# Optimization experiments

Measured on AMD Instinct MI355X. Metric: run time of the kernel, lower is better.

The kernel has to match this reference:

```python
import jax, jax.numpy as jnp
import numpy as np

DIM = 768
HEADS = 12
HIDDEN = 4 * DIM
EPS = 1e-5


def _layernorm(x, g, b):
    mu = jnp.mean(x, axis=-1, keepdims=True)
    var = jnp.var(x, axis=-1, keepdims=True)
    return (x - mu) * jax.lax.rsqrt(var + EPS) * g + b


def setup_inputs() -> dict:
    key = jax.random.key(0)
    ks = jax.random.split(key, 8)
    B, N, C = 16, 577, DIM
    s = lambda fan: 1.0 / np.sqrt(fan)
    return {
        "x": jax.random.normal(ks[0], (B, N, C), jnp.float32),
        "ln1_g": jnp.ones((C,), jnp.float32),
        "ln1_b": jnp.zeros((C,), jnp.float32),
        "qkv_w": jax.random.normal(ks[1], (C, 3 * C), jnp.float32) * s(C),
        "qkv_b": jnp.zeros((3 * C,), jnp.float32),
        "proj_w": jax.random.normal(ks[2], (C, C), jnp.float32) * s(C),
        "proj_b": jnp.zeros((C,), jnp.float32),
        "ln2_g": jnp.ones((C,), jnp.float32),
        "ln2_b": jnp.zeros((C,), jnp.float32),
        "fc1_w": jax.random.normal(ks[3], (C, HIDDEN), jnp.float32) * s(C),
        "fc1_b": jnp.zeros((HIDDEN,), jnp.float32),
        "fc2_w": jax.random.normal(ks[4], (HIDDEN, C), jnp.float32) * s(HIDDEN),
        "fc2_b": jnp.zeros((C,), jnp.float32),
    }


def reference(x, ln1_g, ln1_b, qkv_w, qkv_b, proj_w, proj_b,
              ln2_g, ln2_b, fc1_w, fc1_b, fc2_w, fc2_b):
    B, N, C = x.shape
    H = HEADS
    Dh = C // H
    scale = Dh ** (-0.5)

    # --- attention branch (pre-norm) ---
    xn = _layernorm(x, ln1_g, ln1_b)
    qkv = xn @ qkv_w + qkv_b                         # [B,N,3C]
    qkv = qkv.reshape(B, N, 3, H, Dh).transpose(2, 0, 3, 1, 4)  # [3,B,H,N,Dh]
    q, k, v = qkv[0], qkv[1], qkv[2]
    attn = jax.nn.softmax(jnp.einsum('bhnd,bhmd->bhnm', q, k) * scale, axis=-1)
    y = jnp.einsum('bhnm,bhmd->bhnd', attn, v)       # [B,H,N,Dh]
    y = y.transpose(0, 2, 1, 3).reshape(B, N, C)
    y = y @ proj_w + proj_b
    x = x + y

    # --- MLP branch (pre-norm, exact GELU as torch default) ---
    xn2 = _layernorm(x, ln2_g, ln2_b)
    h = jax.nn.gelu(xn2 @ fc1_w + fc1_b, approximate=False)
    x = x + (h @ fc2_w + fc2_b)
    return x
```

## Files before the change

### kernel.cpp

```cpp
#include <hip/hip_runtime.h>
#include <hip/hip_bf16.h>
#include <math.h>


#define C_DIM   768
#define SEQ     577
#define BATCH   16
#define NHEAD   12
#define DHEAD   64
#define MREAL   (BATCH*SEQ)
#define MPAD    9472
#define HID     3072
#define QKW     1536
#define NKV     640
#define QSCALE  0.1803368801111204f

typedef __hip_bfloat16 bf16;
typedef __attribute__((ext_vector_type(8))) short v8s;
typedef __attribute__((ext_vector_type(4))) float v4f;
typedef __attribute__((ext_vector_type(16))) float v16f;

static __device__ __forceinline__ bf16 f2b(float f){ return __float2bfloat16(f); }
static __device__ __forceinline__ float us2f(unsigned short u){
  union{ float f; unsigned int i; } x; x.i = ((unsigned int)u)<<16; return x.f;
}
static __device__ __forceinline__ short f2s(float f){
  bf16 t = __float2bfloat16(f); return *(short*)&t;
}
static __device__ __forceinline__ float gelu_fast(float x){
  float z2 = 2.302585092994046f * x * (1.f + 0.044715f*x*x);
  return x / (1.f + exp2f(-z2));
}

__global__ __launch_bounds__(256) void k_transpose_all(
    const float* __restrict__ qkvw, const float* __restrict__ projw,
    const float* __restrict__ fc1w, const float* __restrict__ fc2w,
    bf16* __restrict__ qkvT, bf16* __restrict__ projT,
    bf16* __restrict__ fc1T, bf16* __restrict__ fc2T)
{
  int id = blockIdx.x;
  const float* src; bf16* dst; int R, C, nx;
  if (id < 432)      { src=qkvw; dst=qkvT; R=768;  C=2304; nx=36; }
  else if (id < 576) { id-=432; src=projw; dst=projT; R=768;  C=768;  nx=12; }
  else if (id < 1152){ id-=576; src=fc1w;  dst=fc1T;  R=768;  C=3072; nx=48; }
  else               { id-=1152; src=fc2w; dst=fc2T;  R=3072; C=768;  nx=12; }
  const int tr = (id/nx)*64, tc = (id%nx)*64;

  __shared__ float s[64][65];
  const int t = threadIdx.x;
  const int lr = t >> 4, lc4 = t & 15;
  #pragma unroll
  for (int i=0;i<4;i++){
    int r = lr + i*16;
    float4 v = *(const float4*)(src + (size_t)(tr+r)*C + tc + lc4*4);
    s[r][lc4*4+0]=v.x; s[r][lc4*4+1]=v.y; s[r][lc4*4+2]=v.z; s[r][lc4*4+3]=v.w;
  }
  __syncthreads();
  const int c = t >> 2, seg = t & 3;
  alignas(16) bf16 tmp[16];
  #pragma unroll
  for (int j=0;j<16;j++) tmp[j] = f2b(s[seg*16+j][c]);
  bf16* dp = dst + (size_t)(tc+c)*R + tr + seg*16;
  *(uint4*)dp       = *(uint4*)tmp;
  *(uint4*)(dp + 8) = *(uint4*)(tmp + 8);
}

__global__ __launch_bounds__(256) void k_layernorm(
    const float* __restrict__ in, const float* __restrict__ g,
    const float* __restrict__ b, bf16* __restrict__ o)
{
  int row = blockIdx.x, tid = threadIdx.x;
  size_t base = (size_t)row*C_DIM;
  if (row >= MREAL){
    #pragma unroll
    for (int j=0;j<3;j++) o[base + tid + j*256] = f2b(0.f);
    return;
  }
  float v[3], s=0.f, ss=0.f;
  #pragma unroll
  for (int j=0;j<3;j++){ v[j] = in[base + tid + j*256]; s += v[j]; ss += v[j]*v[j]; }
  #pragma unroll
  for (int off=32; off>0; off>>=1){ s += __shfl_xor(s,off); ss += __shfl_xor(ss,off); }
  __shared__ float red[8];
  int wv = tid>>6;
  if ((tid&63)==0){ red[wv] = s; red[4+wv] = ss; }
  __syncthreads();
  float S  = red[0]+red[1]+red[2]+red[3];
  float SS = red[4]+red[5]+red[6]+red[7];
  float mu   = S*(1.f/C_DIM);
  float rstd = rsqrtf(SS*(1.f/C_DIM) - mu*mu + 1e-5f);
  #pragma unroll
  for (int j=0;j<3;j++){
    int c = tid + j*256;
    o[base+c] = f2b((v[j]-mu)*rstd*g[c] + b[c]);
  }
}

__global__ __launch_bounds__(256) void k_reduce2_ln(
    const bf16* __restrict__ P, const float* __restrict__ bias,
    const float* __restrict__ resid, float* __restrict__ out,
    const float* __restrict__ g, const float* __restrict__ bln,
    bf16* __restrict__ xn2)
{
  int row = blockIdx.x, tid = threadIdx.x;
  size_t base = (size_t)row*C_DIM;
  if (row >= MREAL){
    #pragma unroll
    for (int j=0;j<3;j++) xn2[base + tid + j*256] = f2b(0.f);
    return;
  }
  const unsigned short* P0 = (const unsigned short*)P;
  const unsigned short* P1 = P0 + (size_t)MPAD*C_DIM;
  float v[3], s=0.f, ss=0.f;
  #pragma unroll
  for (int j=0;j<3;j++){
    int c = tid + j*256;
    size_t idx = base + c;
    float val = us2f(P0[idx]) + us2f(P1[idx]) + bias[c] + resid[idx];
    out[idx] = val; v[j] = val; s += val; ss += val*val;
  }
  #pragma unroll
  for (int off=32; off>0; off>>=1){ s += __shfl_xor(s,off); ss += __shfl_xor(ss,off); }
  __shared__ float red[8];
  int wv = tid>>6;
  if ((tid&63)==0){ red[wv] = s; red[4+wv] = ss; }
  __syncthreads();
  float S  = red[0]+red[1]+red[2]+red[3];
  float SS = red[4]+red[5]+red[6]+red[7];
  float mu   = S*(1.f/C_DIM);
  float rstd = rsqrtf(SS*(1.f/C_DIM) - mu*mu + 1e-5f);
  #pragma unroll
  for (int j=0;j<3;j++){
    int c = tid + j*256;
    xn2[base+c] = f2b((v[j]-mu)*rstd*g[c] + bln[c]);
  }
}

__global__ __launch_bounds__(256) void k_reduce2(
    const bf16* __restrict__ P, const float* __restrict__ bias,
    const float* __restrict__ resid, float* __restrict__ out)
{
  size_t i = ((size_t)blockIdx.x*256 + threadIdx.x)*8;
  int c = (int)(i % C_DIM);
  v8s p0 = *(const v8s*)(P + i);
  v8s p1 = *(const v8s*)(P + (size_t)MPAD*C_DIM + i);
  float r[8];
  #pragma unroll
  for (int j=0;j<8;j++) r[j] = resid[i+j];
  #pragma unroll
  for (int j=0;j<8;j++)
    out[i+j] = us2f((unsigned short)p0[j]) + us2f((unsigned short)p1[j])
             + bias[c+j] + r[j];
}

__global__ __launch_bounds__(256, 3) void k_flash(
    const bf16* __restrict__ qk, const bf16* __restrict__ VtAll,
    bf16* __restrict__ y)
{
  __shared__ alignas(16) bf16 sK[2][64*64];
  __shared__ alignas(16) bf16 sV[2][64*64];
  __shared__ alignas(16) bf16 sP[4][16*72];

  const int tid = threadIdx.x;
  const int wave = tid>>6, lane = tid&63;
  const int r16 = lane&15, kg = lane>>4;

  const int id = blockIdx.x;
  const int swz = (id&7)*240 + (id>>3);
  const int hh = swz/10, qt = swz - hh*10;
  const int b_ = hh/NHEAD, h_ = hh - b_*NHEAD;

  const int qrow = b_*SEQ + qt*64 + wave*16 + r16;
  v8s qf[2];
  qf[0] = *(const v8s*)(qk + (size_t)qrow*QKW + h_*DHEAD + kg*8);
  qf[1] = *(const v8s*)(qk + (size_t)qrow*QKW + h_*DHEAD + 32 + kg*8);

  auto stage = [&](int kt, int buf){
    #pragma unroll
    for (int i=0;i<2;i++){
      int chunk = i*256 + tid;
      int row = chunk>>3, ch = chunk&7;
      int sc = ch ^ (row&7);
      const bf16* gk = qk + (size_t)(b_*SEQ + kt*64 + row)*QKW
                          + C_DIM + h_*DHEAD + sc*8;
      const bf16* gv = VtAll + (size_t)(b_*C_DIM + h_*DHEAD + row)*NKV
                             + kt*64 + sc*8;
      __builtin_amdgcn_global_load_lds(
          (const __attribute__((address_space(1))) void*)gk,
          (__attribute__((address_space(3))) void*)((char*)&sK[buf][0] + i*4096 + wave*1024),
          16, 0, 0);
      __builtin_amdgcn_global_load_lds(
          (const __attribute__((address_space(1))) void*)gv,
          (__attribute__((address_space(3))) void*)((char*)&sV[buf][0] + i*4096 + wave*1024),
          16, 0, 0);
    }
  };

  float m_run = -1e30f, l_run = 0.f;
  v4f zero4 = {0.f,0.f,0.f,0.f};
  v4f o[4] = {zero4, zero4, zero4, zero4};

  stage(0, 0);
  for (int kt=0; kt<10; ++kt){
    __syncthreads();
    if (kt < 9) stage(kt+1, (kt+1)&1);
    const bf16* Kt = &sK[kt&1][0];
    const bf16* Vt = &sV[kt&1][0];

    v4f sfr[4] = {zero4, zero4, zero4, zero4};
    #pragma unroll
    for (int ks=0; ks<2; ++ks){
      #pragma unroll
      for (int m=0;m<4;m++){
        int key = m*16 + r16;
        v8s kf = *(const v8s*)(Kt + key*64 + (((ks*4+kg) ^ (key&7))*8));
        sfr[m] = __builtin_amdgcn_mfma_f32_16x16x32_bf16(kf, qf[ks], sfr[m], 0, 0, 0);
      }
    }

    if (kt == 9){
      #pragma unroll
      for (int m=0;m<4;m++)
        #pragma unroll
        for (int gg=0; gg<4; ++gg){
          int kb = 576 + m*16 + kg*4 + gg;
          if (kb >= SEQ) sfr[m][gg] = -1e30f;
        }
    }

    float tmax = -1e30f;
    #pragma unroll
    for (int m=0;m<4;m++)
      #pragma unroll
      for (int gg=0; gg<4; ++gg) tmax = fmaxf(tmax, sfr[m][gg]);
    tmax = fmaxf(tmax, __shfl_xor(tmax, 16));
    tmax = fmaxf(tmax, __shfl_xor(tmax, 32));
    float mn  = fmaxf(m_run, tmax);
    float scl = exp2f(m_run - mn);
    float ps  = 0.f;
    #pragma unroll
    for (int m=0;m<4;m++)
      #pragma unroll
      for (int gg=0; gg<4; ++gg){
        float pv = exp2f(sfr[m][gg] - mn);
        sfr[m][gg] = pv; ps += pv;
      }
    ps += __shfl_xor(ps, 16);
    ps += __shfl_xor(ps, 32);
    l_run = l_run*scl + ps;
    m_run = mn;
    #pragma unroll
    for (int mf=0; mf<4; ++mf) o[mf] *= scl;

    bf16* Pw = &sP[wave][0];
    #pragma unroll
    for (int m=0;m<4;m++){
      short4 w;
      w.x = f2s(sfr[m][0]); w.y = f2s(sfr[m][1]);
      w.z = f2s(sfr[m][2]); w.w = f2s(sfr[m][3]);
      *(short4*)(Pw + r16*72 + m*16 + kg*4) = w;
    }
    asm volatile("s_waitcnt lgkmcnt(0)" ::: "memory");
    v8s pb0 = *(const v8s*)(Pw + r16*72 + kg*8);
    v8s pb1 = *(const v8s*)(Pw + r16*72 + 32 + kg*8);
    #pragma unroll
    for (int mf=0; mf<4; ++mf){
      int d = mf*16 + r16;
      v8s v0 = *(const v8s*)(Vt + d*64 + ((kg     ^ (d&7))*8));
      v8s v1 = *(const v8s*)(Vt + d*64 + (((4+kg) ^ (d&7))*8));
      o[mf] = __builtin_amdgcn_mfma_f32_16x16x32_bf16(v0, pb0, o[mf], 0, 0, 0);
      o[mf] = __builtin_amdgcn_mfma_f32_16x16x32_bf16(v1, pb1, o[mf], 0, 0, 0);
    }
  }

  const int qg = qt*64 + wave*16 + r16;
  if (qg < SEQ){
    float inv = 1.f / l_run;
    #pragma unroll
    for (int mf=0; mf<4; ++mf){
      short4 w;
      w.x = f2s(o[mf][0]*inv); w.y = f2s(o[mf][1]*inv);
      w.z = f2s(o[mf][2]*inv); w.w = f2s(o[mf][3]*inv);
      *(short4*)(y + (size_t)(b_*SEQ + qg)*C_DIM + h_*DHEAD + mf*16 + kg*4) = w;
    }
  }
}

template<int EPI>
__global__ __launch_bounds__(256, 4) void gemm_bt(
    const bf16* __restrict__ A, int lda,
    const bf16* __restrict__ BT, int ldb,
    void* Cv, int ldc,
    const float* __restrict__ bias,
    const float* resid,
    int K)
{
  __shared__ alignas(16) bf16 sA[128*64];
  __shared__ alignas(16) bf16 sB[128*64];
  const int tid  = threadIdx.x;
  const int wave = tid>>6, lane = tid&63;
  const int wr = wave>>1, wc = wave&1;
  const int r16 = lane&15, kg = lane>>4;

  int nx = gridDim.x, nwg = nx*gridDim.y;
  int id = blockIdx.y*nx + blockIdx.x;
  int qq = nwg>>3, r8 = nwg&7, xcd = id&7, j = id>>3;
  int swz = (xcd<r8 ? xcd*(qq+1) : r8*(qq+1) + (xcd-r8)*qq) + j;
  int mt = swz / nx, nt = swz % nx;

  int kb = 0;
  if constexpr (EPI==6) kb = blockIdx.z * K;

  v4f acc[4][4];
  v4f zero4 = {0.f,0.f,0.f,0.f};
  #pragma unroll
  for (int m=0;m<4;m++)
    #pragma unroll
    for (int n=0;n<4;n++) acc[m][n] = zero4;

  const int mrow0 = mt*128, ncol0 = nt*128;

  for (int kt=0; kt<K; kt+=64){
    #pragma unroll
    for (int i=0;i<4;i++){
      int ci = wave*4 + i;
      int q  = ci*64 + lane;
      int rr = q>>3;
      int cc = (q&7)*8;
      const bf16* ga = A  + (size_t)(mrow0+rr)*lda + (kb+kt+cc);
      const bf16* gb = BT + (size_t)(ncol0+rr)*ldb + (kb+kt+cc);
      __builtin_amdgcn_global_load_lds(
          (const __attribute__((address_space(1))) void*)ga,
          (__attribute__((address_space(3))) void*)((char*)sA + ci*1024), 16, 0, 0);
      __builtin_amdgcn_global_load_lds(
          (const __attribute__((address_space(1))) void*)gb,
          (__attribute__((address_space(3))) void*)((char*)sB + ci*1024), 16, 0, 0);
    }
    __syncthreads();
    #pragma unroll
    for (int ks=0; ks<2; ks++){
      v8s av[4], bv[4];
      #pragma unroll
      for (int m=0;m<4;m++)
        av[m] = *(const v8s*)(sA + (wr*64 + m*16 + r16)*64 + ks*32 + kg*8);
      #pragma unroll
      for (int n=0;n<4;n++)
        bv[n] = *(const v8s*)(sB + (wc*64 + n*16 + r16)*64 + ks*32 + kg*8);
      #pragma unroll
      for (int m=0;m<4;m++)
        #pragma unroll
        for (int n=0;n<4;n++)
          acc[m][n] = __builtin_amdgcn_mfma_f32_16x16x32_bf16(av[m], bv[n], acc[m][n], 0, 0, 0);
    }
    __syncthreads();
  }

  #pragma unroll
  for (int m=0;m<4;m++){
    #pragma unroll
    for (int n=0;n<4;n++){
      int col = ncol0 + wc*64 + n*16 + r16;
      #pragma unroll
      for (int gg=0; gg<4; gg++){
        int row = mrow0 + wr*64 + m*16 + kg*4 + gg;
        float v = acc[m][n][gg];
        if constexpr (EPI==0){
          float oo = v + bias[col];
          if (col < C_DIM) oo *= QSCALE;
          ((bf16*)Cv)[(size_t)row*ldc + col] = f2b(oo);
        } else if constexpr (EPI==5){
          int g = col;
          if (g < MREAL){
            int b = g / SEQ;
            int key = g - b*SEQ;
            ((bf16*)Cv)[((size_t)b*C_DIM + row)*NKV + key] = f2b(v + bias[row]);
          }
        } else {
          ((bf16*)Cv)[(size_t)blockIdx.z*MPAD*C_DIM + (size_t)row*ldc + col] = f2b(v);
        }
      }
    }
  }
}

__global__ __launch_bounds__(256, 4) void gemm_bt32(
    const bf16* __restrict__ A, int lda,
    const bf16* __restrict__ BT, int ldb,
    bf16* __restrict__ Cv, int ldc,
    const float* __restrict__ bias,
    int K)
{
  __shared__ alignas(16) bf16 sA[128*64];
  __shared__ alignas(16) bf16 sB[128*64];
  const int tid  = threadIdx.x;
  const int wave = tid>>6, lane = tid&63;
  const int wr = wave>>1, wc = wave&1;
  const int l31 = lane&31, lh = lane>>5;

  int nx = gridDim.x, nwg = nx*gridDim.y;
  int id = blockIdx.y*nx + blockIdx.x;
  int qq = nwg>>3, r8 = nwg&7, xcd = id&7, j = id>>3;
  int swz = (xcd<r8 ? xcd*(qq+1) : r8*(qq+1) + (xcd-r8)*qq) + j;
  int mt = swz / nx, nt = swz % nx;
  const int mrow0 = mt*128, ncol0 = nt*128;

  v16f acc[2][2];
  #pragma unroll
  for (int i=0;i<2;i++)
    #pragma unroll
    for (int jn=0;jn<2;jn++)
      #pragma unroll
      for (int r=0;r<16;r++) acc[i][jn][r] = 0.f;

  for (int kt=0; kt<K; kt+=64){
    #pragma unroll
    for (int i=0;i<4;i++){
      int ci = wave*4 + i;
      int q  = ci*64 + lane;
      int rr = q>>3;
      int cc = (q&7)*8;
      const bf16* ga = A  + (size_t)(mrow0+rr)*lda + (kt+cc);
      const bf16* gb = BT + (size_t)(ncol0+rr)*ldb + (kt+cc);
      __builtin_amdgcn_global_load_lds(
          (const __attribute__((address_space(1))) void*)ga,
          (__attribute__((address_space(3))) void*)((char*)sA + ci*1024), 16, 0, 0);
      __builtin_amdgcn_global_load_lds(
          (const __attribute__((address_space(1))) void*)gb,
          (__attribute__((address_space(3))) void*)((char*)sB + ci*1024), 16, 0, 0);
    }
    __syncthreads();
    #pragma unroll
    for (int ks=0; ks<4; ks++){
      v8s a[2], b[2];
      #pragma unroll
      for (int i=0;i<2;i++)
        a[i] = *(const v8s*)(sA + (wr*64 + i*32 + l31)*64 + ks*16 + lh*8);
      #pragma unroll
      for (int jn=0;jn<2;jn++)
        b[jn] = *(const v8s*)(sB + (wc*64 + jn*32 + l31)*64 + ks*16 + lh*8);
      #pragma unroll
      for (int i=0;i<2;i++)
        #pragma unroll
        for (int jn=0;jn<2;jn++)
          acc[i][jn] = __builtin_amdgcn_mfma_f32_32x32x16_bf16(a[i], b[jn], acc[i][jn], 0, 0, 0);
    }
    __syncthreads();
  }

  #pragma unroll
  for (int i=0;i<2;i++){
    #pragma unroll
    for (int jn=0;jn<2;jn++){
      int col = ncol0 + wc*64 + jn*32 + l31;
      float bcol = bias[col];
      #pragma unroll
      for (int r=0;r<16;r++){
        int row = mrow0 + wr*64 + i*32 + (r&3) + 8*(r>>2) + 4*lh;
        Cv[(size_t)row*ldc + col] = f2b(gelu_fast(acc[i][jn][r] + bcol));
      }
    }
  }
}


extern "C" void kernel_launch(void* const* d_in, const int* in_sizes, int n_in,
                              void* d_out, int out_size, void* d_ws, size_t ws_size,
                              hipStream_t stream)
{
  const float* x     = (const float*)d_in[0];
  const float* ln1g  = (const float*)d_in[1];
  const float* ln1b  = (const float*)d_in[2];
  const float* qkvw  = (const float*)d_in[3];
  const float* qkvb  = (const float*)d_in[4];
  const float* projw = (const float*)d_in[5];
  const float* projb = (const float*)d_in[6];
  const float* ln2g  = (const float*)d_in[7];
  const float* ln2b  = (const float*)d_in[8];
  const float* fc1w  = (const float*)d_in[9];
  const float* fc1b  = (const float*)d_in[10];
  const float* fc2w  = (const float*)d_in[11];
  const float* fc2b  = (const float*)d_in[12];
  float* out = (float*)d_out;

  char* p = (char*)d_ws;
  auto take = [&](size_t n){ char* r = p; p += (n + 255) & ~(size_t)255; return r; };
  bf16* qkvT = (bf16*)take((size_t)(3*C_DIM)*C_DIM*2);
  bf16* projT= (bf16*)take((size_t)C_DIM*C_DIM*2);
  bf16* fc1T = (bf16*)take((size_t)HID*C_DIM*2);
  bf16* fc2T = (bf16*)take((size_t)C_DIM*HID*2);
  bf16* xn   = (bf16*)take((size_t)MPAD*C_DIM*2);
  bf16* xn2  = (bf16*)take((size_t)MPAD*C_DIM*2);
  bf16* qk   = (bf16*)take((size_t)MPAD*QKW*2);
  bf16* y    = (bf16*)take((size_t)MPAD*C_DIM*2);
  bf16* h    = (bf16*)take((size_t)MPAD*HID*2);
  bf16* VtAll= (bf16*)take((size_t)(BATCH*C_DIM + 2*DHEAD)*NKV*2);
  bf16* P    = qk;

  k_transpose_all<<<1728, 256, 0, stream>>>(qkvw, projw, fc1w, fc2w,
                                            qkvT, projT, fc1T, fc2T);

  k_layernorm<<<MPAD, 256, 0, stream>>>(x, ln1g, ln1b, xn);

  gemm_bt<0><<<dim3(QKW/128, MPAD/128), 256, 0, stream>>>(
      xn, C_DIM, qkvT, C_DIM, qk, QKW, qkvb, nullptr, C_DIM);

  gemm_bt<5><<<dim3(MPAD/128, C_DIM/128), 256, 0, stream>>>(
      qkvT + (size_t)QKW*C_DIM, C_DIM, xn, C_DIM, VtAll, 0,
      qkvb + 2*C_DIM, nullptr, C_DIM);

  k_flash<<<1920, 256, 0, stream>>>(qk, VtAll, y);

  gemm_bt<6><<<dim3(C_DIM/128, MPAD/128, 2), 256, 0, stream>>>(
      y, C_DIM, projT, C_DIM, P, C_DIM, nullptr, nullptr, C_DIM/2);
  k_reduce2_ln<<<MPAD, 256, 0, stream>>>(P, projb, x, out, ln2g, ln2b, xn2);

  gemm_bt32<<<dim3(HID/128, MPAD/128), 256, 0, stream>>>(
      xn2, C_DIM, fc1T, C_DIM, h, HID, fc1b, C_DIM);

  gemm_bt<6><<<dim3(C_DIM/128, MPAD/128, 2), 256, 0, stream>>>(
      h, HID, fc2T, HID, P, C_DIM, nullptr, nullptr, HID/2);
  k_reduce2<<<(MREAL*C_DIM)/(256*8), 256, 0, stream>>>(P, fc2b, out, out);
}
```

Before: 319.8 us.

## Replace fc1 GEMM with 8-wave 16x16 MFMA kernel and reuse it for fc2

The 4-wave 32x32x16 MFMA GEMM for fc1 becomes an 8-wave (512-thread) kernel that keeps the same 128x128 tile. Each wave computes a 64x32 sub-tile with 16x16x32 MFMAs, so it holds fewer accumulator registers. The kernel is templated so the split-K fc2 GEMM also uses it instead of the generic gemm_bt. The goal is to hide latency with more waves per CU and lower register pressure, at the cost of more LDS reads per MFMA and a different epilogue write pattern.

```diff
diff --git a/kernel.cpp b/kernel.cpp
--- a/kernel.cpp
+++ b/kernel.cpp
@@ -18,7 +18,6 @@
 typedef __hip_bfloat16 bf16;
 typedef __attribute__((ext_vector_type(8))) short v8s;
 typedef __attribute__((ext_vector_type(4))) float v4f;
-typedef __attribute__((ext_vector_type(16))) float v16f;
 
 static __device__ __forceinline__ bf16 f2b(float f){ return __float2bfloat16(f); }
 static __device__ __forceinline__ float us2f(unsigned short u){
@@ -383,10 +382,11 @@
   }
 }
 
-__global__ __launch_bounds__(256, 4) void gemm_bt32(
+template<int EPI>
+__global__ __launch_bounds__(512, 6) void gemm_bt8(
     const bf16* __restrict__ A, int lda,
     const bf16* __restrict__ BT, int ldb,
-    bf16* __restrict__ Cv, int ldc,
+    void* Cv, int ldc,
     const float* __restrict__ bias,
     int K)
 {
@@ -394,33 +394,36 @@
   __shared__ alignas(16) bf16 sB[128*64];
   const int tid  = threadIdx.x;
   const int wave = tid>>6, lane = tid&63;
-  const int wr = wave>>1, wc = wave&1;
-  const int l31 = lane&31, lh = lane>>5;
+  const int wr = wave>>2, wc = wave&3;
+  const int r16 = lane&15, kg = lane>>4;
 
   int nx = gridDim.x, nwg = nx*gridDim.y;
   int id = blockIdx.y*nx + blockIdx.x;
   int qq = nwg>>3, r8 = nwg&7, xcd = id&7, j = id>>3;
   int swz = (xcd<r8 ? xcd*(qq+1) : r8*(qq+1) + (xcd-r8)*qq) + j;
   int mt = swz / nx, nt = swz % nx;
+
+  int kb = 0;
+  if constexpr (EPI==6) kb = blockIdx.z * K;
+
+  v4f acc[4][2];
+  v4f zero4 = {0.f,0.f,0.f,0.f};
+  #pragma unroll
+  for (int m=0;m<4;m++)
+    #pragma unroll
+    for (int n=0;n<2;n++) acc[m][n] = zero4;
+
   const int mrow0 = mt*128, ncol0 = nt*128;
 
-  v16f acc[2][2];
-  #pragma unroll
-  for (int i=0;i<2;i++)
-    #pragma unroll
-    for (int jn=0;jn<2;jn++)
-      #pragma unroll
-      for (int r=0;r<16;r++) acc[i][jn][r] = 0.f;
-
   for (int kt=0; kt<K; kt+=64){
     #pragma unroll
-    for (int i=0;i<4;i++){
-      int ci = wave*4 + i;
+    for (int i=0;i<2;i++){
+      int ci = wave*2 + i;
       int q  = ci*64 + lane;
       int rr = q>>3;
       int cc = (q&7)*8;
-      const bf16* ga = A  + (size_t)(mrow0+rr)*lda + (kt+cc);
-      const bf16* gb = BT + (size_t)(ncol0+rr)*ldb + (kt+cc);
+      const bf16* ga = A  + (size_t)(mrow0+rr)*lda + (kb+kt+cc);
+      const bf16* gb = BT + (size_t)(ncol0+rr)*ldb + (kb+kt+cc);
       __builtin_amdgcn_global_load_lds(
           (const __attribute__((address_space(1))) void*)ga,
           (__attribute__((address_space(3))) void*)((char*)sA + ci*1024), 16, 0, 0);
@@ -430,33 +433,37 @@
     }
     __syncthreads();
     #pragma unroll
-    for (int ks=0; ks<4; ks++){
-      v8s a[2], b[2];
-      #pragma unroll
-      for (int i=0;i<2;i++)
-        a[i] = *(const v8s*)(sA + (wr*64 + i*32 + l31)*64 + ks*16 + lh*8);
-      #pragma unroll
-      for (int jn=0;jn<2;jn++)
-        b[jn] = *(const v8s*)(sB + (wc*64 + jn*32 + l31)*64 + ks*16 + lh*8);
-      #pragma unroll
-      for (int i=0;i<2;i++)
+    for (int ks=0; ks<2; ks++){
+      v8s av[4], bv[2];
+      #pragma unroll
+      for (int m=0;m<4;m++)
+        av[m] = *(const v8s*)(sA + (wr*64 + m*16 + r16)*64 + ks*32 + kg*8);
+      #pragma unroll
+      for (int n=0;n<2;n++)
+        bv[n] = *(const v8s*)(sB + (wc*32 + n*16 + r16)*64 + ks*32 + kg*8);
+      #pragma unroll
+      for (int m=0;m<4;m++)
         #pragma unroll
-        for (int jn=0;jn<2;jn++)
-          acc[i][jn] = __builtin_amdgcn_mfma_f32_32x32x16_bf16(a[i], b[jn], acc[i][jn], 0, 0, 0);
+        for (int n=0;n<2;n++)
+          acc[m][n] = __builtin_amdgcn_mfma_f32_16x16x32_bf16(av[m], bv[n], acc[m][n], 0, 0, 0);
     }
     __syncthreads();
   }
 
   #pragma unroll
-  for (int i=0;i<2;i++){
-    #pragma unroll
-    for (int jn=0;jn<2;jn++){
-      int col = ncol0 + wc*64 + jn*32 + l31;
-      float bcol = bias[col];
-      #pragma unroll
-      for (int r=0;r<16;r++){
-        int row = mrow0 + wr*64 + i*32 + (r&3) + 8*(r>>2) + 4*lh;
-        Cv[(size_t)row*ldc + col] = f2b(gelu_fast(acc[i][jn][r] + bcol));
+  for (int m=0;m<4;m++){
+    #pragma unroll
+    for (int n=0;n<2;n++){
+      int col = ncol0 + wc*32 + n*16 + r16;
+      #pragma unroll
+      for (int gg=0; gg<4; gg++){
+        int row = mrow0 + wr*64 + m*16 + kg*4 + gg;
+        float v = acc[m][n][gg];
+        if constexpr (EPI==1){
+          ((bf16*)Cv)[(size_t)row*ldc + col] = f2b(gelu_fast(v + bias[col]));
+        } else {
+          ((bf16*)Cv)[(size_t)blockIdx.z*MPAD*C_DIM + (size_t)row*ldc + col] = f2b(v);
+        }
       }
     }
   }
@@ -514,10 +521,10 @@
       y, C_DIM, projT, C_DIM, P, C_DIM, nullptr, nullptr, C_DIM/2);
   k_reduce2_ln<<<MPAD, 256, 0, stream>>>(P, projb, x, out, ln2g, ln2b, xn2);
 
-  gemm_bt32<<<dim3(HID/128, MPAD/128), 256, 0, stream>>>(
+  gemm_bt8<1><<<dim3(HID/128, MPAD/128), 512, 0, stream>>>(
       xn2, C_DIM, fc1T, C_DIM, h, HID, fc1b, C_DIM);
 
-  gemm_bt<6><<<dim3(C_DIM/128, MPAD/128, 2), 256, 0, stream>>>(
-      h, HID, fc2T, HID, P, C_DIM, nullptr, nullptr, HID/2);
+  gemm_bt8<6><<<dim3(C_DIM/128, MPAD/128, 2), 512, 0, stream>>>(
+      h, HID, fc2T, HID, P, C_DIM, nullptr, HID/2);
   k_reduce2<<<(MREAL*C_DIM)/(256*8), 256, 0, stream>>>(P, fc2b, out, out);
 }
```

Result: slower. 330.7 us (+3.4%).
